# Optimization experiments

Hardware: AMD Instinct MI355X
Metric: run time of the kernel (lower is better)

The kernel has to match this reference:

```python
import jax, jax.numpy as jnp
import numpy as np

F = 26          # field_size
D = 16          # embed_dim
B = 16384       # batch
VOCABS = [1000] * F
OFFSETS = np.concatenate([[0], np.cumsum(VOCABS)[:-1]]).astype(np.int32)
IU, JU = np.triu_indices(F, k=1)   # 325 pairs (i<j)
P = IU.shape[0]
BN_EPS = 1e-3   # Keras BatchNormalization default epsilon


def setup_inputs() -> dict:
    key = jax.random.key(0)
    ks = jax.random.split(key, 8)
    s = 0.05  # keras 'random_normal' initializer stddev
    return {
        "x": jax.random.randint(ks[0], (B, F), 0, 1000, dtype=jnp.int32),
        "emb_table": jax.random.normal(ks[1], (sum(VOCABS) + 1, D), jnp.float32) * s,
        "se_w1": jax.random.normal(ks[2], (F, F // 2), jnp.float32) * s,
        "se_w2": jax.random.normal(ks[3], (F // 2, F), jnp.float32) * s,
        "bl_w": jax.random.normal(ks[4], (P, D, D), jnp.float32) * s,
        "w1": jax.random.normal(ks[5], (F * (F - 1) * D, 64), jnp.float32) * s,
        "b1": jnp.zeros((64,), jnp.float32),
        "g1": jnp.ones((64,), jnp.float32),
        "be1": jnp.zeros((64,), jnp.float32),
        "m1": jnp.zeros((64,), jnp.float32),
        "v1": jnp.ones((64,), jnp.float32),
        "w2": jax.random.normal(ks[6], (64, 32), jnp.float32) * s,
        "b2": jnp.zeros((32,), jnp.float32),
        "g2": jnp.ones((32,), jnp.float32),
        "be2": jnp.zeros((32,), jnp.float32),
        "m2": jnp.zeros((32,), jnp.float32),
        "v2": jnp.ones((32,), jnp.float32),
        "w3": jax.random.normal(ks[7], (32, 1), jnp.float32) * s,
        "b3": jnp.zeros((1,), jnp.float32),
    }


def _bilinear(v, bl_w):
    # v: [B, F, D]; shared W stack over the 325 ordered pairs (i<j)
    # tmp[p] = (v_i @ W_p) * v_j  -> [B, P, D]
    return jnp.einsum('bpd,pde->bpe', v[:, IU], bl_w) * v[:, JU]


def _bn(h, g, b, m, v):
    return g * (h - m) * jax.lax.rsqrt(v + BN_EPS) + b


def reference(x, emb_table, se_w1, se_w2, bl_w,
              w1, b1, g1, be1, m1, v1,
              w2, b2, g2, be2, m2, v2,
              w3, b3):
    ids = x + jnp.asarray(OFFSETS)
    e = emb_table[ids]                         # [B, F, D]
    # SE layer: mean-pool over embed dim, two ReLU dense layers, rescale
    z = e.mean(axis=-1)                        # [B, F]
    A = jax.nn.relu(jax.nn.relu(z @ se_w1) @ se_w2)
    se = e * A[..., None]                      # [B, F, D]
    # Bilinear interaction (same weights for both calls)
    p = _bilinear(e, bl_w).reshape(e.shape[0], -1)     # [B, P*D]
    se_p = _bilinear(se, bl_w).reshape(e.shape[0], -1)
    h = jnp.concatenate([p, se_p], axis=-1)    # [B, F*(F-1)*D]
    # MLP with inference-mode BatchNorm; dropout=0 is a no-op
    h = jax.nn.relu(_bn(h @ w1 + b1, g1, be1, m1, v1))
    h = jax.nn.relu(_bn(h @ w2 + b2, g2, be2, m2, v2))
    return jax.nn.sigmoid(h @ w3 + b3)         # [B, 1]
```

## Files before the change

kernel.cpp:

```cpp
#include <hip/hip_runtime.h>
#include <cstdint>
#include <cstddef>


#define F_FIELDS 26
#define P_PAIRS 325
#define PAD_PAIRS 336
#define BATCH 16384
#define BN_EPS 1e-3f
#define ROWS 64

typedef short bf16x8 __attribute__((ext_vector_type(8)));
typedef float f32x4 __attribute__((ext_vector_type(4)));

struct PairTab { unsigned char iu[PAD_PAIRS]; unsigned char ju[PAD_PAIRS]; };
static constexpr PairTab make_pairs() {
    PairTab t{};
    int p = 0;
    for (int a = 0; a < F_FIELDS; ++a)
        for (int b = a + 1; b < F_FIELDS; ++b) { t.iu[p] = (unsigned char)a; t.ju[p] = (unsigned char)b; ++p; }
    for (; p < PAD_PAIRS; ++p) { t.iu[p] = 0; t.ju[p] = 0; }
    return t;
}
__constant__ PairTab PT = make_pairs();

__device__ __forceinline__ unsigned short bf16u(float v) {
    unsigned u = __float_as_uint(v);
    unsigned r = (u + 0x7fffu + ((u >> 16) & 1u)) >> 16;
    return (unsigned short)r;
}
__device__ __forceinline__ unsigned pk_bf16(float lo, float hi) {
    return (unsigned)bf16u(lo) | ((unsigned)bf16u(hi) << 16);
}
__device__ __forceinline__ float bflo(unsigned d) { return __uint_as_float(d << 16); }
__device__ __forceinline__ float bfhi(unsigned d) { return __uint_as_float(d & 0xffff0000u); }
__device__ __forceinline__ unsigned pk_trunc(float u, float cu) {
    return __builtin_amdgcn_perm(__float_as_uint(cu), __float_as_uint(u), 0x07060302u);
}

__global__ __launch_bounds__(256) void k_wprep(const float* __restrict__ w1,
        const float* __restrict__ blw, unsigned short* __restrict__ w1catL,
        unsigned short* __restrict__ wcatL) {
    const int p = blockIdx.x;
    const int tid = threadIdx.x;
    if (p >= P_PAIRS) {
        int4 z = make_int4(0, 0, 0, 0);
        *(int4*)(w1catL + (size_t)p * 2048 + tid * 8) = z;
        if (tid < 64) *(int4*)(wcatL + (size_t)p * 512 + tid * 8) = z;
        return;
    }
    __shared__ float wu[1024], wv[1024], wb[256];
    ((float4*)wu)[tid] = ((const float4*)(w1 + (size_t)p * 1024))[tid];
    ((float4*)wv)[tid] = ((const float4*)(w1 + 332800 + (size_t)p * 1024))[tid];
    if (tid < 64) ((float4*)wb)[tid] = ((const float4*)(blw + (size_t)p * 256))[tid];
    __syncthreads();
    {
        int nt = tid >> 6, lane = tid & 63, ln = lane & 15, q = lane >> 4;
        int o = nt * 16 + ln;
        unsigned short outv[8];
        #pragma unroll
        for (int j = 0; j < 8; ++j) {
            int k = q * 8 + j, d = k >> 1, su = k & 1;
            outv[j] = bf16u(su ? wv[d * 64 + o] : wu[d * 64 + o]);
        }
        *(int4*)(w1catL + (size_t)p * 2048 + tid * 8) = *(const int4*)outv;
    }
    if (tid < 64) {
        int ln = tid & 15, q = tid >> 4;
        unsigned short outv[8];
        #pragma unroll
        for (int j = 0; j < 8; ++j) {
            int din = q * 8 + j;
            outv[j] = (din < 16) ? bf16u(wb[din * 16 + ln]) : (unsigned short)0;
        }
        *(int4*)(wcatL + (size_t)p * 512 + tid * 8) = *(const int4*)outv;
    }
}

union __align__(16) SMem {
    struct {
        unsigned short eS[ROWS * 424];
        float aS[F_FIELDS * ROWS];
    } a;
    struct {
        unsigned ysh[8 * 8 * 64 * 4];
        float h1s[ROWS * 65];
        float h2s[ROWS * 36];
    } b;
};

__global__ __launch_bounds__(512, 2) void k_main(const int* __restrict__ x,
        const float* __restrict__ emb, const float* __restrict__ sw1,
        const float* __restrict__ sw2, const unsigned short* __restrict__ w1catL,
        const unsigned short* __restrict__ wcatL,
        const float* __restrict__ b1, const float* __restrict__ g1,
        const float* __restrict__ be1, const float* __restrict__ m1,
        const float* __restrict__ v1,
        const float* __restrict__ w2, const float* __restrict__ b2,
        const float* __restrict__ g2, const float* __restrict__ be2,
        const float* __restrict__ m2, const float* __restrict__ v2,
        const float* __restrict__ w3, const float* __restrict__ b3,
        float* __restrict__ out) {
    __shared__ SMem sm;
    __shared__ float z_s[ROWS][F_FIELDS];
    __shared__ float sw1_s[F_FIELDS * 13];
    __shared__ float sw2_s[13 * F_FIELDS];
    const int tid = threadIdx.x;
    const int b0 = blockIdx.x * ROWS;
    unsigned short* eS = sm.a.eS;
    float* aS = sm.a.aS;

    for (int i = tid; i < F_FIELDS * 13; i += 512) { sw1_s[i] = sw1[i]; sw2_s[i] = sw2[i]; }
    for (int idx = tid; idx < ROWS * F_FIELDS; idx += 512) {
        int r = idx / F_FIELDS, f = idx - r * F_FIELDS;
        int id = x[(b0 + r) * F_FIELDS + f] + f * 1000;
        const float4* src = (const float4*)(emb + (size_t)id * 16);
        float4 v0 = src[0], v1l = src[1], v2l = src[2], v3l = src[3];
        int4 o0, o1;
        o0.x = (int)pk_bf16(v0.x, v0.y);  o0.y = (int)pk_bf16(v0.z, v0.w);
        o0.z = (int)pk_bf16(v1l.x, v1l.y); o0.w = (int)pk_bf16(v1l.z, v1l.w);
        o1.x = (int)pk_bf16(v2l.x, v2l.y); o1.y = (int)pk_bf16(v2l.z, v2l.w);
        o1.z = (int)pk_bf16(v3l.x, v3l.y); o1.w = (int)pk_bf16(v3l.z, v3l.w);
        *(int4*)(eS + r * 424 + f * 16) = o0;
        *(int4*)(eS + r * 424 + f * 16 + 8) = o1;
        float s = v0.x + v0.y + v0.z + v0.w + v1l.x + v1l.y + v1l.z + v1l.w
                + v2l.x + v2l.y + v2l.z + v2l.w + v3l.x + v3l.y + v3l.z + v3l.w;
        z_s[r][f] = s * (1.0f / 16.0f);
    }
    __syncthreads();
    if (tid < ROWS) {
        float s1[13];
        #pragma unroll
        for (int o = 0; o < 13; ++o) {
            float acc0 = 0.f;
            #pragma unroll
            for (int f = 0; f < F_FIELDS; ++f) acc0 = fmaf(z_s[tid][f], sw1_s[f * 13 + o], acc0);
            s1[o] = fmaxf(acc0, 0.0f);
        }
        #pragma unroll
        for (int f = 0; f < F_FIELDS; ++f) {
            float acc0 = 0.f;
            #pragma unroll
            for (int o = 0; o < 13; ++o) acc0 = fmaf(s1[o], sw2_s[o * F_FIELDS + f], acc0);
            aS[f * ROWS + tid] = fmaxf(acc0, 0.0f);
        }
    }
    __syncthreads();

    const int w    = tid >> 6;
    const int lane = tid & 63;
    const int ln   = lane & 15;
    const int q    = lane >> 4;
    const int p0 = w * 42, p1 = p0 + 42;

    f32x4 acc[4][4];
    #pragma unroll
    for (int a = 0; a < 4; ++a)
        #pragma unroll
        for (int b = 0; b < 4; ++b) acc[a][b] = (f32x4){0.f, 0.f, 0.f, 0.f};
    const f32x4 zero4 = {0.f, 0.f, 0.f, 0.f};

    int iu_c = PT.iu[p0];
    bf16x8 eiB[4];
    float ai[4];
    #pragma unroll
    for (int mt = 0; mt < 4; ++mt) {
        eiB[mt] = __builtin_bit_cast(bf16x8,
            *(const int4*)(eS + (mt * 16 + ln) * 424 + iu_c * 16 + (q & 1) * 8));
        ai[mt] = aS[iu_c * ROWS + mt * 16 + ln];
    }
    bf16x8 wa_c = __builtin_bit_cast(bf16x8, *(const int4*)(wcatL + (size_t)p0 * 512 + lane * 8));
    bf16x8 wb_c[4];
    #pragma unroll
    for (int nt = 0; nt < 4; ++nt)
        wb_c[nt] = __builtin_bit_cast(bf16x8, *(const int4*)(w1catL + (size_t)p0 * 2048 + nt * 512 + lane * 8));
    f32x4 tc[4];
    #pragma unroll
    for (int mt = 0; mt < 4; ++mt)
        tc[mt] = __builtin_amdgcn_mfma_f32_16x16x32_bf16(wa_c, eiB[mt], zero4, 0, 0, 0);

    #pragma unroll 2
    for (int p = p0; p < p1; ++p) {
        const int pn = (p + 1 < p1) ? (p + 1) : p;
        bf16x8 wa_n = __builtin_bit_cast(bf16x8, *(const int4*)(wcatL + (size_t)pn * 512 + lane * 8));
        bf16x8 wb_n[4];
        #pragma unroll
        for (int nt = 0; nt < 4; ++nt)
            wb_n[nt] = __builtin_bit_cast(bf16x8, *(const int4*)(w1catL + (size_t)pn * 2048 + nt * 512 + lane * 8));

        const int ju = PT.ju[p];
        uint2 ejv[4];
        float cv[4];
        #pragma unroll
        for (int mt = 0; mt < 4; ++mt) {
            ejv[mt] = *(const uint2*)(eS + (mt * 16 + ln) * 424 + ju * 16 + q * 4);
            cv[mt]  = ai[mt] * aS[ju * ROWS + mt * 16 + ln];
        }
        const int iu_n = PT.iu[pn];
        if (iu_n != iu_c) {
            iu_c = iu_n;
            #pragma unroll
            for (int mt = 0; mt < 4; ++mt) {
                eiB[mt] = __builtin_bit_cast(bf16x8,
                    *(const int4*)(eS + (mt * 16 + ln) * 424 + iu_c * 16 + (q & 1) * 8));
                ai[mt] = aS[iu_c * ROWS + mt * 16 + ln];
            }
        }

        #pragma unroll
        for (int mt = 0; mt < 4; ++mt) {
            f32x4 t = tc[mt];
            float e0 = bflo(ejv[mt].x), e1 = bfhi(ejv[mt].x);
            float e2 = bflo(ejv[mt].y), e3 = bfhi(ejv[mt].y);
            float c  = cv[mt];
            float u0 = t[0] * e0, u1 = t[1] * e1, u2 = t[2] * e2, u3 = t[3] * e3;
            int4 af;
            af.x = (int)pk_trunc(u0, c * u0);
            af.y = (int)pk_trunc(u1, c * u1);
            af.z = (int)pk_trunc(u2, c * u2);
            af.w = (int)pk_trunc(u3, c * u3);
            bf16x8 A = __builtin_bit_cast(bf16x8, af);
            #pragma unroll
            for (int nt = 0; nt < 4; ++nt)
                acc[mt][nt] = __builtin_amdgcn_mfma_f32_16x16x32_bf16(A, wb_c[nt], acc[mt][nt], 0, 0, 0);
        }
        #pragma unroll
        for (int mt = 0; mt < 4; ++mt)
            tc[mt] = __builtin_amdgcn_mfma_f32_16x16x32_bf16(wa_n, eiB[mt], zero4, 0, 0, 0);
        wa_c = wa_n;
        #pragma unroll
        for (int nt = 0; nt < 4; ++nt) wb_c[nt] = wb_n[nt];
    }

    __syncthreads();
    unsigned* ysh = sm.b.ysh;
    float* h1s = sm.b.h1s;
    float* h2s = sm.b.h2s;
    #pragma unroll
    for (int mt = 0; mt < 4; ++mt)
        #pragma unroll
        for (int nh = 0; nh < 2; ++nh) {
            int nt0 = nh * 2, nt1 = nh * 2 + 1;
            int4 v;
            v.x = (int)pk_bf16(acc[mt][nt0][0], acc[mt][nt0][1]);
            v.y = (int)pk_bf16(acc[mt][nt0][2], acc[mt][nt0][3]);
            v.z = (int)pk_bf16(acc[mt][nt1][0], acc[mt][nt1][1]);
            v.w = (int)pk_bf16(acc[mt][nt1][2], acc[mt][nt1][3]);
            *(int4*)(ysh + ((w * 8 + mt * 2 + nh) * 64 + lane) * 4) = v;
        }
    __syncthreads();

    {
        const int s = tid >> 6, lane2 = tid & 63, ln2 = lane2 & 15, q2 = lane2 >> 4;
        const int mt = s >> 1, nh = s & 1;
        const int c0 = nh * 32 + ln2, c1 = c0 + 16;
        const float sc0 = g1[c0] * rsqrtf(v1[c0] + BN_EPS);
        const float of0 = be1[c0] + sc0 * (b1[c0] - m1[c0]);
        const float sc1 = g1[c1] * rsqrtf(v1[c1] + BN_EPS);
        const float of1 = be1[c1] + sc1 * (b1[c1] - m1[c1]);
        float s8[8];
        #pragma unroll
        for (int i = 0; i < 8; ++i) s8[i] = 0.f;
        #pragma unroll
        for (int wv = 0; wv < 8; ++wv) {
            int4 v = *(const int4*)(ysh + ((wv * 8 + s) * 64 + lane2) * 4);
            s8[0] += bflo((unsigned)v.x); s8[1] += bfhi((unsigned)v.x);
            s8[2] += bflo((unsigned)v.y); s8[3] += bfhi((unsigned)v.y);
            s8[4] += bflo((unsigned)v.z); s8[5] += bfhi((unsigned)v.z);
            s8[6] += bflo((unsigned)v.w); s8[7] += bfhi((unsigned)v.w);
        }
        const int row0 = mt * 16 + q2 * 4;
        #pragma unroll
        for (int r = 0; r < 4; ++r) {
            h1s[(row0 + r) * 65 + c0] = fmaxf(s8[r] * sc0 + of0, 0.f);
            h1s[(row0 + r) * 65 + c1] = fmaxf(s8[4 + r] * sc1 + of1, 0.f);
        }
    }
    __syncthreads();

    {
        const int row = tid >> 3, gg = tid & 7;
        const int o0 = gg * 4;
        float a0 = 0.f, a1 = 0.f, a2 = 0.f, a3 = 0.f;
        #pragma unroll 8
        for (int k = 0; k < 64; ++k) {
            float hk = h1s[row * 65 + k];
            float4 wv = *(const float4*)(w2 + k * 32 + o0);
            a0 = fmaf(hk, wv.x, a0);
            a1 = fmaf(hk, wv.y, a1);
            a2 = fmaf(hk, wv.z, a2);
            a3 = fmaf(hk, wv.w, a3);
        }
        const float4 g2v  = *(const float4*)(g2 + o0);
        const float4 b2v  = *(const float4*)(b2 + o0);
        const float4 m2v  = *(const float4*)(m2 + o0);
        const float4 v2v  = *(const float4*)(v2 + o0);
        const float4 be2v = *(const float4*)(be2 + o0);
        float4 hv;
        hv.x = fmaxf(g2v.x * (a0 + b2v.x - m2v.x) * rsqrtf(v2v.x + BN_EPS) + be2v.x, 0.f);
        hv.y = fmaxf(g2v.y * (a1 + b2v.y - m2v.y) * rsqrtf(v2v.y + BN_EPS) + be2v.y, 0.f);
        hv.z = fmaxf(g2v.z * (a2 + b2v.z - m2v.z) * rsqrtf(v2v.z + BN_EPS) + be2v.z, 0.f);
        hv.w = fmaxf(g2v.w * (a3 + b2v.w - m2v.w) * rsqrtf(v2v.w + BN_EPS) + be2v.w, 0.f);
        *(float4*)(h2s + row * 36 + o0) = hv;
    }
    __syncthreads();
    if (tid < ROWS) {
        float sacc = b3[0];
        #pragma unroll
        for (int k = 0; k < 32; ++k) sacc = fmaf(h2s[tid * 36 + k], w3[k], sacc);
        out[b0 + tid] = 1.0f / (1.0f + expf(-sacc));
    }
}

extern "C" void kernel_launch(void* const* d_in, const int* in_sizes, int n_in,
                              void* d_out, int out_size, void* d_ws, size_t ws_size,
                              hipStream_t stream) {
    const int*   x   = (const int*)d_in[0];
    const float* emb = (const float*)d_in[1];
    const float* sw1 = (const float*)d_in[2];
    const float* sw2 = (const float*)d_in[3];
    const float* blw = (const float*)d_in[4];
    const float* w1  = (const float*)d_in[5];
    const float* b1  = (const float*)d_in[6];
    const float* g1  = (const float*)d_in[7];
    const float* be1 = (const float*)d_in[8];
    const float* m1  = (const float*)d_in[9];
    const float* v1  = (const float*)d_in[10];
    const float* w2  = (const float*)d_in[11];
    const float* b2  = (const float*)d_in[12];
    const float* g2  = (const float*)d_in[13];
    const float* be2 = (const float*)d_in[14];
    const float* m2  = (const float*)d_in[15];
    const float* v2  = (const float*)d_in[16];
    const float* w3  = (const float*)d_in[17];
    const float* b3  = (const float*)d_in[18];
    float* out = (float*)d_out;

    char* ws = (char*)d_ws;
    unsigned short* w1catL = (unsigned short*)ws;
    unsigned short* wcatL  = (unsigned short*)(ws + 1376256);

    hipLaunchKernelGGL(k_wprep, dim3(PAD_PAIRS), dim3(256), 0, stream, w1, blw, w1catL, wcatL);
    hipLaunchKernelGGL(k_main,  dim3(BATCH / ROWS), dim3(512), 0, stream,
                       x, emb, sw1, sw2, w1catL, wcatL,
                       b1, g1, be1, m1, v1, w2, b2, g2, be2, m2, v2, w3, b3, out);
}
```

Baseline: 136.6 us.

## Prefetch bilinear and W1 weights two pairs ahead with explicit inline-asm loads

```diff
diff --git a/kernel.cpp b/kernel.cpp
--- a/kernel.cpp
+++ b/kernel.cpp
@@ -12,6 +12,7 @@
 
 typedef short bf16x8 __attribute__((ext_vector_type(8)));
 typedef float f32x4 __attribute__((ext_vector_type(4)));
+typedef int   i32x4 __attribute__((ext_vector_type(4)));
 
 struct PairTab { unsigned char iu[PAD_PAIRS]; unsigned char ju[PAD_PAIRS]; };
 static constexpr PairTab make_pairs() {
@@ -88,6 +89,61 @@
         float h2s[ROWS * 36];
     } b;
 };
+
+#define ISSUE_W(pp, waS, wbS0, wbS1, wbS2, wbS3) do {                                   \
+    const unsigned short* ba_ = wcatL + (size_t)(pp) * 512 + lane * 8;                  \
+    const unsigned short* bb_ = w1catL + (size_t)(pp) * 2048 + lane * 8;                \
+    asm volatile("global_load_dwordx4 %0, %1, off"             : "=v"(waS)  : "v"(ba_)); \
+    asm volatile("global_load_dwordx4 %0, %1, off"             : "=v"(wbS0) : "v"(bb_)); \
+    asm volatile("global_load_dwordx4 %0, %1, off offset:1024" : "=v"(wbS1) : "v"(bb_)); \
+    asm volatile("global_load_dwordx4 %0, %1, off offset:2048" : "=v"(wbS2) : "v"(bb_)); \
+    asm volatile("global_load_dwordx4 %0, %1, off offset:3072" : "=v"(wbS3) : "v"(bb_)); \
+} while (0)
+
+#define PAIR_BODY(p_, waS, wbS0, wbS1, wbS2, wbS3, waT, wbT0, wbT1, wbT2, wbT3) do {    \
+    const int pn_ = ((p_) + 1 < p1) ? (p_) + 1 : (p1 - 1);                              \
+    const int pf_ = ((p_) + 2 < p1) ? (p_) + 2 : (p1 - 1);                              \
+    const int ju_ = PT.ju[p_];                                                          \
+    uint2 ejv_[4]; float cv_[4];                                                        \
+    _Pragma("unroll") for (int mt = 0; mt < 4; ++mt) {                                  \
+        ejv_[mt] = *(const uint2*)(eS + (mt * 16 + ln) * 424 + ju_ * 16 + q * 4);       \
+        cv_[mt]  = ai[mt] * aS[ju_ * ROWS + mt * 16 + ln];                              \
+    }                                                                                   \
+    const int iun_ = PT.iu[pn_];                                                        \
+    if (iun_ != iu_c) {                                                                 \
+        iu_c = iun_;                                                                    \
+        _Pragma("unroll") for (int mt = 0; mt < 4; ++mt) {                              \
+            eiB[mt] = __builtin_bit_cast(bf16x8,                                        \
+                *(const int4*)(eS + (mt * 16 + ln) * 424 + iu_c * 16 + (q & 1) * 8));   \
+            ai[mt] = aS[iu_c * ROWS + mt * 16 + ln];                                    \
+        }                                                                               \
+    }                                                                                   \
+    bf16x8 wbv_[4] = { __builtin_bit_cast(bf16x8, wbS0), __builtin_bit_cast(bf16x8, wbS1), \
+                       __builtin_bit_cast(bf16x8, wbS2), __builtin_bit_cast(bf16x8, wbS3) }; \
+    _Pragma("unroll") for (int mt = 0; mt < 4; ++mt) {                                  \
+        f32x4 t = tc[mt];                                                               \
+        float e0 = bflo(ejv_[mt].x), e1 = bfhi(ejv_[mt].x);                             \
+        float e2 = bflo(ejv_[mt].y), e3 = bfhi(ejv_[mt].y);                             \
+        float c  = cv_[mt];                                                             \
+        float u0 = t[0] * e0, u1 = t[1] * e1, u2 = t[2] * e2, u3 = t[3] * e3;           \
+        int4 af;                                                                        \
+        af.x = (int)pk_trunc(u0, c * u0);                                               \
+        af.y = (int)pk_trunc(u1, c * u1);                                               \
+        af.z = (int)pk_trunc(u2, c * u2);                                               \
+        af.w = (int)pk_trunc(u3, c * u3);                                               \
+        bf16x8 A_ = __builtin_bit_cast(bf16x8, af);                                     \
+        _Pragma("unroll") for (int nt = 0; nt < 4; ++nt)                                \
+            acc[mt][nt] = __builtin_amdgcn_mfma_f32_16x16x32_bf16(A_, wbv_[nt], acc[mt][nt], 0, 0, 0); \
+    }                                                                                   \
+    ISSUE_W(pf_, waS, wbS0, wbS1, wbS2, wbS3);                                          \
+    asm volatile("s_waitcnt vmcnt(5)" ::: "memory");                                    \
+    __builtin_amdgcn_sched_barrier(0);                                                  \
+    {                                                                                   \
+        bf16x8 waT_ = __builtin_bit_cast(bf16x8, waT);                                  \
+        _Pragma("unroll") for (int mt = 0; mt < 4; ++mt)                                \
+            tc[mt] = __builtin_amdgcn_mfma_f32_16x16x32_bf16(waT_, eiB[mt], zero4, 0, 0, 0); \
+    }                                                                                   \
+} while (0)
 
 __global__ __launch_bounds__(512, 2) void k_main(const int* __restrict__ x,
         const float* __restrict__ emb, const float* __restrict__ sw1,
@@ -169,68 +225,28 @@
             *(const int4*)(eS + (mt * 16 + ln) * 424 + iu_c * 16 + (q & 1) * 8));
         ai[mt] = aS[iu_c * ROWS + mt * 16 + ln];
     }
-    bf16x8 wa_c = __builtin_bit_cast(bf16x8, *(const int4*)(wcatL + (size_t)p0 * 512 + lane * 8));
-    bf16x8 wb_c[4];
-    #pragma unroll
-    for (int nt = 0; nt < 4; ++nt)
-        wb_c[nt] = __builtin_bit_cast(bf16x8, *(const int4*)(w1catL + (size_t)p0 * 2048 + nt * 512 + lane * 8));
+
+    i32x4 waA, wbA0, wbA1, wbA2, wbA3;
+    i32x4 waB, wbB0, wbB1, wbB2, wbB3;
+    ISSUE_W(p0,     waA, wbA0, wbA1, wbA2, wbA3);
+    ISSUE_W(p0 + 1, waB, wbB0, wbB1, wbB2, wbB3);
+    asm volatile("s_waitcnt vmcnt(5)" ::: "memory");
+    __builtin_amdgcn_sched_barrier(0);
+
     f32x4 tc[4];
-    #pragma unroll
-    for (int mt = 0; mt < 4; ++mt)
-        tc[mt] = __builtin_amdgcn_mfma_f32_16x16x32_bf16(wa_c, eiB[mt], zero4, 0, 0, 0);
-
-    #pragma unroll 2
-    for (int p = p0; p < p1; ++p) {
-        const int pn = (p + 1 < p1) ? (p + 1) : p;
-        bf16x8 wa_n = __builtin_bit_cast(bf16x8, *(const int4*)(wcatL + (size_t)pn * 512 + lane * 8));
-        bf16x8 wb_n[4];
-        #pragma unroll
-        for (int nt = 0; nt < 4; ++nt)
-            wb_n[nt] = __builtin_bit_cast(bf16x8, *(const int4*)(w1catL + (size_t)pn * 2048 + nt * 512 + lane * 8));
-
-        const int ju = PT.ju[p];
-        uint2 ejv[4];
-        float cv[4];
-        #pragma unroll
-        for (int mt = 0; mt < 4; ++mt) {
-            ejv[mt] = *(const uint2*)(eS + (mt * 16 + ln) * 424 + ju * 16 + q * 4);
-            cv[mt]  = ai[mt] * aS[ju * ROWS + mt * 16 + ln];
-        }
-        const int iu_n = PT.iu[pn];
-        if (iu_n != iu_c) {
-            iu_c = iu_n;
-            #pragma unroll
-            for (int mt = 0; mt < 4; ++mt) {
-                eiB[mt] = __builtin_bit_cast(bf16x8,
-                    *(const int4*)(eS + (mt * 16 + ln) * 424 + iu_c * 16 + (q & 1) * 8));
-                ai[mt] = aS[iu_c * ROWS + mt * 16 + ln];
-            }
-        }
-
-        #pragma unroll
-        for (int mt = 0; mt < 4; ++mt) {
-            f32x4 t = tc[mt];
-            float e0 = bflo(ejv[mt].x), e1 = bfhi(ejv[mt].x);
-            float e2 = bflo(ejv[mt].y), e3 = bfhi(ejv[mt].y);
-            float c  = cv[mt];
-            float u0 = t[0] * e0, u1 = t[1] * e1, u2 = t[2] * e2, u3 = t[3] * e3;
-            int4 af;
-            af.x = (int)pk_trunc(u0, c * u0);
-            af.y = (int)pk_trunc(u1, c * u1);
-            af.z = (int)pk_trunc(u2, c * u2);
-            af.w = (int)pk_trunc(u3, c * u3);
-            bf16x8 A = __builtin_bit_cast(bf16x8, af);
-            #pragma unroll
-            for (int nt = 0; nt < 4; ++nt)
-                acc[mt][nt] = __builtin_amdgcn_mfma_f32_16x16x32_bf16(A, wb_c[nt], acc[mt][nt], 0, 0, 0);
-        }
+    {
+        bf16x8 waA_ = __builtin_bit_cast(bf16x8, waA);
         #pragma unroll
         for (int mt = 0; mt < 4; ++mt)
-            tc[mt] = __builtin_amdgcn_mfma_f32_16x16x32_bf16(wa_n, eiB[mt], zero4, 0, 0, 0);
-        wa_c = wa_n;
-        #pragma unroll
-        for (int nt = 0; nt < 4; ++nt) wb_c[nt] = wb_n[nt];
-    }
+            tc[mt] = __builtin_amdgcn_mfma_f32_16x16x32_bf16(waA_, eiB[mt], zero4, 0, 0, 0);
+    }
+
+    for (int p = p0; p < p1; p += 2) {
+        PAIR_BODY(p,     waA, wbA0, wbA1, wbA2, wbA3, waB, wbB0, wbB1, wbB2, wbB3);
+        PAIR_BODY(p + 1, waB, wbB0, wbB1, wbB2, wbB3, waA, wbA0, wbA1, wbA2, wbA3);
+    }
+    asm volatile("s_waitcnt vmcnt(0)" ::: "memory");
+    __builtin_amdgcn_sched_barrier(0);
 
     __syncthreads();
     unsigned* ysh = sm.b.ysh;
```

New measurement: 137.2 us. About the same (+0.5%).
